# Kernel tuning notes

Measured on AMD Instinct MI355X. Metric: run time of the kernel, lower is better.

## Reference

```python
import jax, jax.numpy as jnp
import numpy as np

N_ATOMS = 131072
NUM_GS = 128
HIDDEN = 512
N_MOL = 1024


def setup_inputs() -> dict:
    key = jax.random.key(0)
    ks = jax.random.split(key, 16)
    Gs = jax.random.normal(ks[0], (N_ATOMS, NUM_GS), dtype=jnp.float32)
    types = jax.random.randint(ks[1], (N_ATOMS,), 0, 2, dtype=jnp.int32)
    mol_id = jnp.sort(jax.random.randint(ks[2], (N_ATOMS,), 0, N_MOL, dtype=jnp.int32))

    def dense(k, fi, fo):
        return (jax.random.normal(k, (fi, fo), dtype=jnp.float32) / np.float32(np.sqrt(fi)))

    params = {}
    for i, t in enumerate(("A", "B")):
        base = 3 + i * 3
        params[f"W1_{t}"] = dense(ks[base], NUM_GS, HIDDEN)
        params[f"b1_{t}"] = jnp.zeros((HIDDEN,), jnp.float32)
        params[f"W2_{t}"] = dense(ks[base + 1], HIDDEN, HIDDEN)
        params[f"b2_{t}"] = jnp.zeros((HIDDEN,), jnp.float32)
        params[f"W3_{t}"] = dense(ks[base + 2], HIDDEN, 1)
        params[f"b3_{t}"] = jnp.zeros((1,), jnp.float32)
        params[f"off_{t}"] = jnp.zeros((1,), jnp.float32)
    return {"Gs": Gs, "types": types, "mol_id": mol_id, **params}


def _ann(G, W1, b1, W2, b2, W3, b3, off):
    # Atomic NN: two tanh hidden layers, linear scalar output + trainable offset
    h = jnp.tanh(G @ W1 + b1)
    h = jnp.tanh(h @ W2 + b2)
    return (h @ W3 + b3 + off)[:, 0]  # [N]


def reference(Gs, types, mol_id,
              W1_A, b1_A, W2_A, b2_A, W3_A, b3_A, off_A,
              W1_B, b1_B, W2_B, b2_B, W3_B, b3_B, off_B):
    # Per-type expert MLPs; dense-select is the math-equivalent of
    # dynamic_partition -> per-type ANN -> dynamic_stitch for 2 experts.
    eA = _ann(Gs, W1_A, b1_A, W2_A, b2_A, W3_A, b3_A, off_A)
    eB = _ann(Gs, W1_B, b1_B, W2_B, b2_B, W3_B, b3_B, off_B)
    atom_e = jnp.where(types == 0, eA, eB)  # [N_ATOMS]
    # Ragged per-molecule reduce_sum == segment_sum over sorted mol ids
    mol_e = jax.ops.segment_sum(atom_e, mol_id, num_segments=N_MOL)
    counts = jax.ops.segment_sum(jnp.ones_like(atom_e), mol_id, num_segments=N_MOL)
    energy_per_atom = mol_e / jnp.maximum(counts, 1.0)
    return energy_per_atom[:, None]  # [N_MOL, 1]
```

## Files before the change

kernel.cpp:

```cpp
#include <hip/hip_runtime.h>

typedef _Float16 half8  __attribute__((ext_vector_type(8)));
typedef _Float16 half4  __attribute__((ext_vector_type(4)));
typedef float    floatx4 __attribute__((ext_vector_type(4)));

#define N_ATOMS 131072
#define NUM_GS  128
#define HIDDEN  512
#define N_MOL   1024

#define BM      32
#define NB_SIDE (N_ATOMS / BM)
#define NT_TOT  (HIDDEN / 16)
#define SH1_LD  (HIDDEN + 8)

#define WS_CNT_OFF     0
#define WS_MOLSUM_OFF  1024
#define WS_PERM_OFF    9216
#define WS_W1FA_OFF    533504
#define WS_W1FB_OFF    664576
#define WS_W2FA_OFF    795648
#define WS_W2FB_OFF    1319936
#define WS_ZERO_BYTES  5120

__device__ __forceinline__ float fast_tanh(float x) {
    x = fminf(20.f, fmaxf(-20.f, x));
    float e = __expf(2.f * x);
    return (e - 1.f) / (e + 1.f);
}

__global__ __launch_bounds__(256)
void prep_kernel(const int* __restrict__ types,
                 const float* __restrict__ W1A, const float* __restrict__ W1B,
                 const float* __restrict__ W2A, const float* __restrict__ W2B,
                 int* __restrict__ cnt, int* __restrict__ perm,
                 _Float16* __restrict__ W1FA, _Float16* __restrict__ W1FB,
                 _Float16* __restrict__ W2FA, _Float16* __restrict__ W2FB) {
    __shared__ float tile[32][65];
    const int p   = blockIdx.x;
    const int tid = threadIdx.x;

    if (p < 512) {
        __shared__ int sCA[4];
        __shared__ int sBaseA, sBaseB;
        const int i    = p * 256 + tid;
        const int lane = tid & 63;
        const int w    = tid >> 6;
        const bool isA = (types[i] == 0);
        unsigned long long mask = __ballot(isA);
        unsigned long long lt   = ((unsigned long long)1 << lane) - 1;
        int rA = __popcll(mask & lt);
        if (lane == 0) sCA[w] = __popcll(mask);
        __syncthreads();
        if (tid == 0) {
            int tot = sCA[0] + sCA[1] + sCA[2] + sCA[3];
            sBaseA = atomicAdd(&cnt[0], tot);
            sBaseB = atomicAdd(&cnt[1], 256 - tot);
        }
        __syncthreads();
        int preA = 0;
        #pragma unroll
        for (int k = 0; k < 4; ++k) preA += (k < w) ? sCA[k] : 0;
        int preB = w * 64 - preA;
        int rB   = lane - rA;
        if (isA) perm[sBaseA + preA + rA] = i;
        else     perm[N_ATOMS - 1 - (sBaseB + preB + rB)] = i;
        return;
    }

    const float* src; _Float16* dst; int pb;
    if (p < 544)      { src = W1A; dst = W1FA; pb = p - 512; }
    else if (p < 576) { src = W1B; dst = W1FB; pb = p - 544; }
    else if (p < 704) { src = W2A; dst = W2FA; pb = p - 576; }
    else              { src = W2B; dst = W2FB; pb = p - 704; }
    const int bx = pb & 7;
    const int by = pb >> 3;
    const int n0 = bx * 64, k0 = by * 32;
    #pragma unroll
    for (int i = 0; i < 8; ++i) {
        int idx = tid + i * 256;
        int r = idx >> 6, c = idx & 63;
        tile[r][c] = src[(size_t)(k0 + r) * HIDDEN + n0 + c];
    }
    __syncthreads();
    const int nt_l = tid >> 6, lane = tid & 63;
    const int l15 = lane & 15, q = lane >> 4;
    half8 v;
    #pragma unroll
    for (int j = 0; j < 8; ++j)
        v[j] = (_Float16)tile[q * 8 + j][nt_l * 16 + l15];
    const int ntile = bx * 4 + nt_l;
    *(half8*)(dst + (((size_t)by * NT_TOT + ntile) * 64 + lane) * 8) = v;
}

__global__ __launch_bounds__(256, 3)
void mlp_kernel(const float* __restrict__ Gs,
                const int*   __restrict__ mol_id,
                const _Float16* __restrict__ W1FA, const _Float16* __restrict__ W2FA,
                const float* __restrict__ b1A, const float* __restrict__ b2A,
                const float* __restrict__ W3A, const float* __restrict__ b3A,
                const float* __restrict__ offA,
                const _Float16* __restrict__ W1FB, const _Float16* __restrict__ W2FB,
                const float* __restrict__ b1B, const float* __restrict__ b2B,
                const float* __restrict__ W3B, const float* __restrict__ b3B,
                const float* __restrict__ offB,
                const int* __restrict__ cnt, const int* __restrict__ perm,
                float* __restrict__ mol_sum) {
    __shared__ __align__(16) _Float16 sGh[BM][NUM_GS + 8];
    __shared__ __align__(16) _Float16 sH1[BM][SH1_LD];
    __shared__ int   sOrig[BM];
    __shared__ float sPart[4][BM];

    const int b     = blockIdx.x;
    const int nA    = cnt[0];
    const int sideB = (b >= NB_SIDE) ? 1 : 0;
    const int r0    = (sideB ? b - NB_SIDE : b) * BM;
    const int nSide = sideB ? (N_ATOMS - nA) : nA;
    if (r0 >= nSide) return;

    const _Float16 *W1F, *W2F;
    const float *b1, *b2, *W3;
    float b3off;
    if (!sideB) { W1F = W1FA; W2F = W2FA; b1 = b1A; b2 = b2A; W3 = W3A; b3off = b3A[0] + offA[0]; }
    else        { W1F = W1FB; W2F = W2FB; b1 = b1B; b2 = b2B; W3 = W3B; b3off = b3B[0] + offB[0]; }

    const int tid = threadIdx.x;
    if (tid < BM) {
        int r = r0 + tid;
        int orig = -1;
        if (r < nSide) orig = sideB ? perm[N_ATOMS - 1 - r] : perm[r];
        sOrig[tid] = orig;
    }
    __syncthreads();

    #pragma unroll
    for (int i = 0; i < 4; ++i) {
        int idx = tid + 256 * i;
        int row = idx >> 5;
        int c4  = idx & 31;
        int orig = sOrig[row];
        float4 v = make_float4(0.f, 0.f, 0.f, 0.f);
        if (orig >= 0) v = ((const float4*)(Gs + (size_t)orig * NUM_GS))[c4];
        half4 h; h[0] = (_Float16)v.x; h[1] = (_Float16)v.y;
                 h[2] = (_Float16)v.z; h[3] = (_Float16)v.w;
        *(half4*)&sGh[row][c4 * 4] = h;
    }
    __syncthreads();

    const int lane = tid & 63;
    const int wid  = tid >> 6;
    const int l15  = lane & 15;
    const int quad = lane >> 4;

    floatx4 acc[2][8];
    #pragma unroll
    for (int mt = 0; mt < 2; ++mt)
        #pragma unroll
        for (int nt = 0; nt < 8; ++nt) acc[mt][nt] = (floatx4){0.f, 0.f, 0.f, 0.f};

    #pragma unroll
    for (int ks = 0; ks < NUM_GS / 32; ++ks) {
        half8 a0 = *(const half8*)&sGh[l15][ks * 32 + quad * 8];
        half8 a1 = *(const half8*)&sGh[l15 + 16][ks * 32 + quad * 8];
        #pragma unroll
        for (int nt = 0; nt < 8; ++nt) {
            int ntile = wid * 8 + nt;
            half8 bf = *(const half8*)(W1F + (((size_t)ks * NT_TOT + ntile) * 64 + lane) * 8);
            acc[0][nt] = __builtin_amdgcn_mfma_f32_16x16x32_f16(a0, bf, acc[0][nt], 0, 0, 0);
            acc[1][nt] = __builtin_amdgcn_mfma_f32_16x16x32_f16(a1, bf, acc[1][nt], 0, 0, 0);
        }
    }
    #pragma unroll
    for (int nt = 0; nt < 8; ++nt) {
        int col = wid * 128 + nt * 16 + l15;
        float b1v = b1[col];
        #pragma unroll
        for (int mt = 0; mt < 2; ++mt)
            #pragma unroll
            for (int r = 0; r < 4; ++r)
                sH1[mt * 16 + quad * 4 + r][col] = (_Float16)fast_tanh(acc[mt][nt][r] + b1v);
    }
    __syncthreads();

    #pragma unroll
    for (int mt = 0; mt < 2; ++mt)
        #pragma unroll
        for (int nt = 0; nt < 8; ++nt) acc[mt][nt] = (floatx4){0.f, 0.f, 0.f, 0.f};

    #pragma unroll 4
    for (int ks = 0; ks < HIDDEN / 32; ++ks) {
        half8 a0 = *(const half8*)&sH1[l15][ks * 32 + quad * 8];
        half8 a1 = *(const half8*)&sH1[l15 + 16][ks * 32 + quad * 8];
        #pragma unroll
        for (int nt = 0; nt < 8; ++nt) {
            int ntile = wid * 8 + nt;
            half8 bf = *(const half8*)(W2F + (((size_t)ks * NT_TOT + ntile) * 64 + lane) * 8);
            acc[0][nt] = __builtin_amdgcn_mfma_f32_16x16x32_f16(a0, bf, acc[0][nt], 0, 0, 0);
            acc[1][nt] = __builtin_amdgcn_mfma_f32_16x16x32_f16(a1, bf, acc[1][nt], 0, 0, 0);
        }
    }

    float p[2][4];
    #pragma unroll
    for (int mt = 0; mt < 2; ++mt)
        #pragma unroll
        for (int r = 0; r < 4; ++r) p[mt][r] = 0.f;

    #pragma unroll
    for (int nt = 0; nt < 8; ++nt) {
        int col = wid * 128 + nt * 16 + l15;
        float b2v = b2[col];
        float w3v = W3[col];
        #pragma unroll
        for (int mt = 0; mt < 2; ++mt)
            #pragma unroll
            for (int r = 0; r < 4; ++r)
                p[mt][r] += fast_tanh(acc[mt][nt][r] + b2v) * w3v;
    }
    #pragma unroll
    for (int mt = 0; mt < 2; ++mt)
        #pragma unroll
        for (int r = 0; r < 4; ++r) {
            float v = p[mt][r];
            v += __shfl_xor(v, 1, 64);
            v += __shfl_xor(v, 2, 64);
            v += __shfl_xor(v, 4, 64);
            v += __shfl_xor(v, 8, 64);
            p[mt][r] = v;
        }
    if (l15 == 0) {
        #pragma unroll
        for (int mt = 0; mt < 2; ++mt)
            #pragma unroll
            for (int r = 0; r < 4; ++r)
                sPart[wid][mt * 16 + quad * 4 + r] = p[mt][r];
    }
    __syncthreads();
    if (tid < BM) {
        int orig = sOrig[tid];
        if (orig >= 0) {
            float e = sPart[0][tid] + sPart[1][tid] + sPart[2][tid] + sPart[3][tid] + b3off;
            atomicAdd(&mol_sum[mol_id[orig]], e);
        }
    }
}

__global__ void finalize_kernel(const float* __restrict__ mol_sum,
                                const int* __restrict__ mol_id,
                                float* __restrict__ out) {
    int m = blockIdx.x * blockDim.x + threadIdx.x;
    if (m >= N_MOL) return;
    int lo0 = 0, hi0 = N_ATOMS;
    while (lo0 < hi0) { int mid = (lo0 + hi0) >> 1; if (mol_id[mid] < m) lo0 = mid + 1; else hi0 = mid; }
    int lo1 = lo0, hi1 = N_ATOMS;
    while (lo1 < hi1) { int mid = (lo1 + hi1) >> 1; if (mol_id[mid] < m + 1) lo1 = mid + 1; else hi1 = mid; }
    float c = (float)(lo1 - lo0);
    out[m] = mol_sum[m] / fmaxf(c, 1.0f);
}

extern "C" void kernel_launch(void* const* d_in, const int* in_sizes, int n_in,
                              void* d_out, int out_size, void* d_ws, size_t ws_size,
                              hipStream_t stream) {
    const float* Gs     = (const float*)d_in[0];
    const int*   types  = (const int*)d_in[1];
    const int*   mol_id = (const int*)d_in[2];
    const float* W1A = (const float*)d_in[3];
    const float* b1A = (const float*)d_in[4];
    const float* W2A = (const float*)d_in[5];
    const float* b2A = (const float*)d_in[6];
    const float* W3A = (const float*)d_in[7];
    const float* b3A = (const float*)d_in[8];
    const float* oA  = (const float*)d_in[9];
    const float* W1B = (const float*)d_in[10];
    const float* b1B = (const float*)d_in[11];
    const float* W2B = (const float*)d_in[12];
    const float* b2B = (const float*)d_in[13];
    const float* W3B = (const float*)d_in[14];
    const float* b3B = (const float*)d_in[15];
    const float* oB  = (const float*)d_in[16];

    char* ws = (char*)d_ws;
    int*      cnt     = (int*)(ws + WS_CNT_OFF);
    float*    mol_sum = (float*)(ws + WS_MOLSUM_OFF);
    int*      perm    = (int*)(ws + WS_PERM_OFF);
    _Float16* W1FA    = (_Float16*)(ws + WS_W1FA_OFF);
    _Float16* W1FB    = (_Float16*)(ws + WS_W1FB_OFF);
    _Float16* W2FA    = (_Float16*)(ws + WS_W2FA_OFF);
    _Float16* W2FB    = (_Float16*)(ws + WS_W2FB_OFF);
    float* out = (float*)d_out;

    hipMemsetAsync(d_ws, 0, WS_ZERO_BYTES, stream);
    prep_kernel<<<832, 256, 0, stream>>>(types, W1A, W1B, W2A, W2B,
                                         cnt, perm,
                                         W1FA, W1FB, W2FA, W2FB);
    mlp_kernel<<<2 * NB_SIDE, 256, 0, stream>>>(
        Gs, mol_id,
        W1FA, W2FA, b1A, b2A, W3A, b3A, oA,
        W1FB, W2FB, b1B, b2B, W3B, b3B, oB,
        cnt, perm, mol_sum);
    finalize_kernel<<<(N_MOL + 255) / 256, 256, 0, stream>>>(mol_sum, mol_id, out);
}
```

Baseline: 299.0 us.

## Load Gs fragments directly into MFMA registers, cheaper tanh, raise occupancy

Removes the shared-memory staging of the gathered Gs rows: each lane loads its fp32 A-fragment straight from global memory and packs it to fp16 with cvt_pkrtz before the first-layer MFMAs. This drops one barrier and the sGh buffer. Freeing that LDS, together with raising the launch-bounds occupancy hint from 3 to 4 blocks, is meant to allow more resident waves. tanh is rewritten as exp2 plus a hardware reciprocal with no clamping, and the final tanh*W3 accumulation uses an explicit fma. The risks are that every wave (4 per block) now reloads the same Gs rows, so global traffic rises, and that round-toward-zero conversion changes numerics slightly.

```diff
diff --git a/kernel.cpp b/kernel.cpp
--- a/kernel.cpp
+++ b/kernel.cpp
@@ -1,7 +1,7 @@
 #include <hip/hip_runtime.h>
 
 typedef _Float16 half8  __attribute__((ext_vector_type(8)));
-typedef _Float16 half4  __attribute__((ext_vector_type(4)));
+typedef __fp16   fp16x2 __attribute__((ext_vector_type(2)));
 typedef float    floatx4 __attribute__((ext_vector_type(4)));
 
 #define N_ATOMS 131072
@@ -24,9 +24,9 @@
 #define WS_ZERO_BYTES  5120
 
 __device__ __forceinline__ float fast_tanh(float x) {
-    x = fminf(20.f, fmaxf(-20.f, x));
-    float e = __expf(2.f * x);
-    return (e - 1.f) / (e + 1.f);
+    float e = exp2f(x * 2.8853900817779268f);
+    float r = __builtin_amdgcn_rcpf(e + 1.0f);
+    return fmaf(-2.0f, r, 1.0f);
 }
 
 __global__ __launch_bounds__(256)
@@ -93,7 +93,7 @@
     *(half8*)(dst + (((size_t)by * NT_TOT + ntile) * 64 + lane) * 8) = v;
 }
 
-__global__ __launch_bounds__(256, 3)
+__global__ __launch_bounds__(256, 4)
 void mlp_kernel(const float* __restrict__ Gs,
                 const int*   __restrict__ mol_id,
                 const _Float16* __restrict__ W1FA, const _Float16* __restrict__ W2FA,
@@ -106,7 +106,6 @@
                 const float* __restrict__ offB,
                 const int* __restrict__ cnt, const int* __restrict__ perm,
                 float* __restrict__ mol_sum) {
-    __shared__ __align__(16) _Float16 sGh[BM][NUM_GS + 8];
     __shared__ __align__(16) _Float16 sH1[BM][SH1_LD];
     __shared__ int   sOrig[BM];
     __shared__ float sPart[4][BM];
@@ -133,25 +132,16 @@
     }
     __syncthreads();
 
-    #pragma unroll
-    for (int i = 0; i < 4; ++i) {
-        int idx = tid + 256 * i;
-        int row = idx >> 5;
-        int c4  = idx & 31;
-        int orig = sOrig[row];
-        float4 v = make_float4(0.f, 0.f, 0.f, 0.f);
-        if (orig >= 0) v = ((const float4*)(Gs + (size_t)orig * NUM_GS))[c4];
-        half4 h; h[0] = (_Float16)v.x; h[1] = (_Float16)v.y;
-                 h[2] = (_Float16)v.z; h[3] = (_Float16)v.w;
-        *(half4*)&sGh[row][c4 * 4] = h;
-    }
-    __syncthreads();
-
     const int lane = tid & 63;
     const int wid  = tid >> 6;
     const int l15  = lane & 15;
     const int quad = lane >> 4;
 
+    int rowA = sOrig[l15];      if (rowA < 0) rowA = 0;
+    int rowB = sOrig[l15 + 16]; if (rowB < 0) rowB = 0;
+    const float* gA = Gs + (size_t)rowA * NUM_GS + quad * 8;
+    const float* gB = Gs + (size_t)rowB * NUM_GS + quad * 8;
+
     floatx4 acc[2][8];
     #pragma unroll
     for (int mt = 0; mt < 2; ++mt)
@@ -160,14 +150,25 @@
 
     #pragma unroll
     for (int ks = 0; ks < NUM_GS / 32; ++ks) {
-        half8 a0 = *(const half8*)&sGh[l15][ks * 32 + quad * 8];
-        half8 a1 = *(const half8*)&sGh[l15 + 16][ks * 32 + quad * 8];
+        float4 fa0 = *(const float4*)(gA + ks * 32);
+        float4 fa1 = *(const float4*)(gA + ks * 32 + 4);
+        float4 fb0 = *(const float4*)(gB + ks * 32);
+        float4 fb1 = *(const float4*)(gB + ks * 32 + 4);
+        union { half8 h8; fp16x2 h2[4]; } a0u, a1u;
+        a0u.h2[0] = __builtin_amdgcn_cvt_pkrtz(fa0.x, fa0.y);
+        a0u.h2[1] = __builtin_amdgcn_cvt_pkrtz(fa0.z, fa0.w);
+        a0u.h2[2] = __builtin_amdgcn_cvt_pkrtz(fa1.x, fa1.y);
+        a0u.h2[3] = __builtin_amdgcn_cvt_pkrtz(fa1.z, fa1.w);
+        a1u.h2[0] = __builtin_amdgcn_cvt_pkrtz(fb0.x, fb0.y);
+        a1u.h2[1] = __builtin_amdgcn_cvt_pkrtz(fb0.z, fb0.w);
+        a1u.h2[2] = __builtin_amdgcn_cvt_pkrtz(fb1.x, fb1.y);
+        a1u.h2[3] = __builtin_amdgcn_cvt_pkrtz(fb1.z, fb1.w);
         #pragma unroll
         for (int nt = 0; nt < 8; ++nt) {
             int ntile = wid * 8 + nt;
             half8 bf = *(const half8*)(W1F + (((size_t)ks * NT_TOT + ntile) * 64 + lane) * 8);
-            acc[0][nt] = __builtin_amdgcn_mfma_f32_16x16x32_f16(a0, bf, acc[0][nt], 0, 0, 0);
-            acc[1][nt] = __builtin_amdgcn_mfma_f32_16x16x32_f16(a1, bf, acc[1][nt], 0, 0, 0);
+            acc[0][nt] = __builtin_amdgcn_mfma_f32_16x16x32_f16(a0u.h8, bf, acc[0][nt], 0, 0, 0);
+            acc[1][nt] = __builtin_amdgcn_mfma_f32_16x16x32_f16(a1u.h8, bf, acc[1][nt], 0, 0, 0);
         }
     }
     #pragma unroll
@@ -214,8 +215,10 @@
         #pragma unroll
         for (int mt = 0; mt < 2; ++mt)
             #pragma unroll
-            for (int r = 0; r < 4; ++r)
-                p[mt][r] += fast_tanh(acc[mt][nt][r] + b2v) * w3v;
+            for (int r = 0; r < 4; ++r) {
+                float t = fast_tanh(acc[mt][nt][r] + b2v);
+                p[mt][r] = fmaf(t, w3v, p[mt][r]);
+            }
     }
     #pragma unroll
     for (int mt = 0; mt < 2; ++mt)
```

Result: slower. 339.3 us (+13.5%).
